# Kernel tuning notes

Measured on AMD Instinct MI355X. Metric: run time of the kernel, lower is better.

## Reference

```python
import jax, jax.numpy as jnp
import numpy as np

N = 262144
LOC_ENC_LEN = 60
NUM_WEIGHTS = 8
INDIM = 32
OUTDIM = 32
HIDDEN = 32
NEG_SLOPE = 0.01  # nn.LeakyReLU default


def _linear_init(key, fan_in, fan_out):
    # torch nn.Linear default: U(-1/sqrt(fan_in), 1/sqrt(fan_in))
    kw, kb = jax.random.split(key)
    bound = 1.0 / np.sqrt(fan_in)
    w = jax.random.uniform(kw, (fan_in, fan_out), jnp.float32, -bound, bound)
    b = jax.random.uniform(kb, (fan_out,), jnp.float32, -bound, bound)
    return w, b


def setup_inputs() -> dict:
    key = jax.random.key(0)
    ks = jax.random.split(key, 10)
    rel_loc_feat = jax.random.normal(ks[0], (N, LOC_ENC_LEN), jnp.float32)
    feat = jax.random.normal(ks[1], (N, INDIM), jnp.float32)
    dims = [LOC_ENC_LEN, HIDDEN, HIDDEN, HIDDEN, HIDDEN, HIDDEN, NUM_WEIGHTS]
    params = {}
    for i in range(6):
        w, b = _linear_init(ks[2 + i], dims[i], dims[i + 1])
        params[f'sn_w{i}'] = w
        params[f'sn_b{i}'] = b
    # weights_bank: kaiming_normal on [num_weights, indim*outdim] -> std = sqrt(2/fan_in), fan_in = indim*outdim
    std = np.sqrt(2.0 / (INDIM * OUTDIM))
    params['bank'] = jax.random.normal(ks[9], (NUM_WEIGHTS, INDIM * OUTDIM), jnp.float32) * std
    return {'rel_loc_feat': rel_loc_feat, 'feat': feat, **params}


def _score_net(x, ws, bs):
    # 5 Linear+LeakyReLU blocks, then final Linear (no activation)
    for i in range(5):
        x = x @ ws[i] + bs[i]
        x = jnp.where(x >= 0, x, NEG_SLOPE * x)
    return x @ ws[5] + bs[5]


def reference(rel_loc_feat, feat,
              sn_w0, sn_b0, sn_w1, sn_b1, sn_w2, sn_b2,
              sn_w3, sn_b3, sn_w4, sn_b4, sn_w5, sn_b5, bank):
    ws = [sn_w0, sn_w1, sn_w2, sn_w3, sn_w4, sn_w5]
    bs = [sn_b0, sn_b1, sn_b2, sn_b3, sn_b4, sn_b5]
    logits = _score_net(rel_loc_feat, ws, bs)          # [N, num_weights]
    coeff = jax.nn.softmax(logits, axis=-1)            # [N, num_weights]
    # per-point weight matrix: [N, indim*outdim] -> [N, indim, outdim]
    weights = (coeff @ bank).reshape(coeff.shape[0], INDIM, OUTDIM)
    # per-point matmul: feat[:, None] @ weights -> squeeze
    out = jnp.einsum('ni,nio->no', feat, weights)      # [N, outdim]
    return out
```

## Files before the change

### kernel.cpp

```cpp
#include <hip/hip_runtime.h>
#include <stdint.h>


typedef __attribute__((ext_vector_type(8))) __bf16 bf16x8;
typedef __attribute__((ext_vector_type(4))) float f32x4;

union FragU { uint32_t u[4]; bf16x8 v; uint4 q; };

__device__ __forceinline__ unsigned short f2bf(float f) {
    union { float f; uint32_t i; } v; v.f = f;
    return (unsigned short)((v.i + 0x7FFFu + ((v.i >> 16) & 1u)) >> 16);
}
__device__ __forceinline__ float bf2f(uint32_t u16) {
    union { uint32_t i; float f; } v; v.i = u16 << 16; return v.f;
}
__device__ __forceinline__ uint32_t pk2(float x, float y) {
    return (uint32_t)f2bf(x) | ((uint32_t)f2bf(y) << 16);
}
__device__ __forceinline__ int permK(int k) {
    return 4 * (k >> 3) + (k & 3) + 16 * ((k >> 2) & 1);
}
__device__ __forceinline__ f32x4 MF(bf16x8 a, bf16x8 b, f32x4 c) {
    return __builtin_amdgcn_mfma_f32_16x16x32_bf16(a, b, c, 0, 0, 0);
}


struct WPf { const float* p[13]; };

__global__ void pc_prep(WPf wp, uint32_t* __restrict__ ws) {
    int idx = blockIdx.x * blockDim.x + threadIdx.x;
    if (idx >= 10240) return;
    if (idx < 7424) {
        int layer, t, chunk = 0, lane, d; const float* w; bool perm;
        int r = idx;
        if (r < 1024) { chunk = r >> 9; r &= 511; t = r >> 8; r &= 255; lane = r >> 2; d = r & 3;
                        layer = 0; w = wp.p[0]; perm = false; }
        else if (r < 3072) { r -= 1024; layer = 1 + (r >> 9); r &= 511; t = r >> 8; r &= 255;
                             lane = r >> 2; d = r & 3; w = wp.p[2 * layer]; perm = true; }
        else if (r < 3328) { r -= 3072; layer = 5; t = 0; lane = r >> 2; d = r & 3;
                             w = wp.p[10]; perm = true; }
        else { r -= 3328; int bk = r >> 9; r &= 511; t = r >> 8; r &= 255; lane = r >> 2; d = r & 3;
               layer = -1; w = wp.p[12] + bk * 1024; perm = false; }
        int gq = lane >> 4, m = t * 16 + (lane & 15);
        uint32_t o = 0;
        #pragma unroll
        for (int e = 0; e < 2; ++e) {
            int kf = 8 * gq + 2 * d + e;
            float v = 0.f;
            if (layer == -1) {
                v = w[kf * 32 + m];
            } else {
                int ks = perm ? permK(kf) : (chunk * 32 + kf);
                if (layer == 0)      { if (ks < 60) v = w[ks * 32 + m]; }
                else if (layer == 5) { if (m < 8)   v = w[ks * 8 + m]; }
                else                 v = w[ks * 32 + m];
            }
            o |= ((uint32_t)f2bf(v)) << (16 * e);
        }
        ws[idx] = o;
    } else if (idx < 9984) {
        int r = idx - 7424; int L = r >> 9; r &= 511; int t = r >> 8; r &= 255;
        int lane = r >> 2, rr = r & 3;
        ((float*)ws)[idx] = wp.p[2 * L + 1][t * 16 + 4 * (lane >> 4) + rr];
    } else {
        int r = idx - 9984; int lane = r >> 2, rr = r & 3;
        int m = 4 * (lane >> 4) + rr;
        ((float*)ws)[idx] = (m < 8) ? wp.p[11][m] : 0.f;
    }
}

#define IT 8

__global__ __launch_bounds__(256, 2) void pc_main(
    const float* __restrict__ rel, const float* __restrict__ feat,
    const uint32_t* __restrict__ wsu, float* __restrict__ out)
{
    const int lane = threadIdx.x & 63;
    const int wv = threadIdx.x >> 6;
    const int g = lane >> 4;
    const int n16 = lane & 15;

    bf16x8 A0[2][2], A14[4][2], A5, AB[8][2];
    f32x4 Bi[5][2], Bi5;
    {
        #pragma unroll
        for (int c = 0; c < 2; ++c)
            #pragma unroll
            for (int t = 0; t < 2; ++t) {
                FragU f; f.q = ((const uint4*)(wsu + (c * 2 + t) * 256))[lane];
                A0[c][t] = f.v;
            }
        #pragma unroll
        for (int L = 0; L < 4; ++L)
            #pragma unroll
            for (int t = 0; t < 2; ++t) {
                FragU f; f.q = ((const uint4*)(wsu + 1024 + L * 512 + t * 256))[lane];
                A14[L][t] = f.v;
            }
        { FragU f; f.q = ((const uint4*)(wsu + 3072))[lane]; A5 = f.v; }
        #pragma unroll
        for (int k = 0; k < 8; ++k)
            #pragma unroll
            for (int t = 0; t < 2; ++t) {
                FragU f; f.q = ((const uint4*)(wsu + 3328 + (k * 2 + t) * 256))[lane];
                AB[k][t] = f.v;
            }
        const float* bw = (const float*)wsu;
        #pragma unroll
        for (int L = 0; L < 5; ++L)
            #pragma unroll
            for (int t = 0; t < 2; ++t) {
                float4 b = ((const float4*)(bw + 7424 + L * 512 + t * 256))[lane];
                Bi[L][t][0] = b.x; Bi[L][t][1] = b.y; Bi[L][t][2] = b.z; Bi[L][t][3] = b.w;
            }
        float4 b = ((const float4*)(bw + 9984))[lane];
        Bi5[0] = b.x; Bi5[1] = b.y; Bi5[2] = b.z; Bi5[3] = b.w;
    }

    const size_t pt0 = (size_t)(blockIdx.x * 4 + wv) * (16 * IT);

    for (int it = 0; it < IT; ++it) {
        const size_t n = pt0 + (size_t)it * 16 + n16;

        const float* rrow = rel + n * 60;
        float4 ra = *(const float4*)(rrow + 8 * g);
        float4 rb = *(const float4*)(rrow + 8 * g + 4);
        float4 rc = *(const float4*)(rrow + 32 + 8 * g);
        float4 rd = make_float4(0.f, 0.f, 0.f, 0.f);
        if (g < 3) rd = *(const float4*)(rrow + 36 + 8 * g);
        FragU b0, b1;
        b0.u[0] = pk2(ra.x, ra.y); b0.u[1] = pk2(ra.z, ra.w);
        b0.u[2] = pk2(rb.x, rb.y); b0.u[3] = pk2(rb.z, rb.w);
        b1.u[0] = pk2(rc.x, rc.y); b1.u[1] = pk2(rc.z, rc.w);
        b1.u[2] = pk2(rd.x, rd.y); b1.u[3] = pk2(rd.z, rd.w);

        f32x4 t0 = Bi[0][0], t1 = Bi[0][1];
        t0 = MF(A0[0][0], b0.v, t0); t1 = MF(A0[0][1], b0.v, t1);
        t0 = MF(A0[1][0], b1.v, t0); t1 = MF(A0[1][1], b1.v, t1);

        #pragma unroll
        for (int L = 0; L < 5; ++L) {
            FragU bx;
            #pragma unroll
            for (int r = 0; r < 4; ++r) {
                t0[r] = fmaxf(t0[r], 0.f) + 0.01f * fminf(t0[r], 0.f);
                t1[r] = fmaxf(t1[r], 0.f) + 0.01f * fminf(t1[r], 0.f);
            }
            bx.u[0] = pk2(t0[0], t0[1]); bx.u[1] = pk2(t0[2], t0[3]);
            bx.u[2] = pk2(t1[0], t1[1]); bx.u[3] = pk2(t1[2], t1[3]);
            if (L < 4) {
                f32x4 n0 = Bi[L + 1][0], n1 = Bi[L + 1][1];
                n0 = MF(A14[L][0], bx.v, n0);
                n1 = MF(A14[L][1], bx.v, n1);
                t0 = n0; t1 = n1;
            } else {
                t0 = MF(A5, bx.v, Bi5);
            }
        }

        float m4 = fmaxf(fmaxf(t0[0], t0[1]), fmaxf(t0[2], t0[3]));
        float m8 = fmaxf(m4, __shfl_xor(m4, 16, 64));
        float e0 = __expf(t0[0] - m8), e1 = __expf(t0[1] - m8);
        float e2 = __expf(t0[2] - m8), e3 = __expf(t0[3] - m8);
        float s4 = e0 + e1 + e2 + e3;
        float s8 = s4 + __shfl_xor(s4, 16, 64);
        float inv = 1.0f / s8;
        uint32_t pc01 = pk2(e0 * inv, e1 * inv);
        uint32_t pc23 = pk2(e2 * inv, e3 * inv);
        uint32_t q01 = (uint32_t)__builtin_amdgcn_ds_bpermute(n16 * 4, (int)pc01);
        uint32_t q23 = (uint32_t)__builtin_amdgcn_ds_bpermute(n16 * 4, (int)pc23);
        uint32_t q45 = (uint32_t)__builtin_amdgcn_ds_bpermute((n16 + 16) * 4, (int)pc01);
        uint32_t q67 = (uint32_t)__builtin_amdgcn_ds_bpermute((n16 + 16) * 4, (int)pc23);
        float cw[8] = { bf2f(q01 & 0xffff), bf2f(q01 >> 16),
                        bf2f(q23 & 0xffff), bf2f(q23 >> 16),
                        bf2f(q45 & 0xffff), bf2f(q45 >> 16),
                        bf2f(q67 & 0xffff), bf2f(q67 >> 16) };

        const float* frow = feat + n * 32 + 8 * g;
        float4 fa = *(const float4*)frow;
        float4 fb = *(const float4*)(frow + 4);
        FragU bf_;
        bf_.u[0] = pk2(fa.x, fa.y); bf_.u[1] = pk2(fa.z, fa.w);
        bf_.u[2] = pk2(fb.x, fb.y); bf_.u[3] = pk2(fb.z, fb.w);

        f32x4 o0 = {0.f, 0.f, 0.f, 0.f}, o1 = {0.f, 0.f, 0.f, 0.f};
        #pragma unroll
        for (int k = 0; k < 8; ++k) {
            f32x4 z = {0.f, 0.f, 0.f, 0.f};
            f32x4 u0 = MF(AB[k][0], bf_.v, z);
            f32x4 u1 = MF(AB[k][1], bf_.v, z);
            #pragma unroll
            for (int r = 0; r < 4; ++r) { o0[r] += cw[k] * u0[r]; o1[r] += cw[k] * u1[r]; }
        }

        float* orow = out + n * 32;
        *(float4*)(orow + 4 * g)      = make_float4(o0[0], o0[1], o0[2], o0[3]);
        *(float4*)(orow + 16 + 4 * g) = make_float4(o1[0], o1[1], o1[2], o1[3]);
    }
}

extern "C" void kernel_launch(void* const* d_in, const int* in_sizes, int n_in,
                              void* d_out, int out_size, void* d_ws, size_t ws_size,
                              hipStream_t stream)
{
    const float* rel = (const float*)d_in[0];
    const float* feat = (const float*)d_in[1];
    WPf wp;
    for (int i = 0; i < 13; ++i) wp.p[i] = (const float*)d_in[2 + i];
    uint32_t* ws = (uint32_t*)d_ws;
    float* out = (float*)d_out;

    const int npts = in_sizes[0] / 60;
    const int nwaves = npts / (16 * IT);
    const int nblocks = nwaves / 4;

    hipLaunchKernelGGL(pc_prep, dim3(40), dim3(256), 0, stream, wp, ws);
    hipLaunchKernelGGL(pc_main, dim3(nblocks), dim3(256), 0, stream, rel, feat, ws, out);
}
```

Measured before the change: 163.2 us.

## Stage weight fragments in LDS and process two 16-point tiles per iteration

```diff
diff --git a/kernel.cpp b/kernel.cpp
--- a/kernel.cpp
+++ b/kernel.cpp
@@ -69,134 +69,168 @@
     }
 }
 
-#define IT 8
+#define IT 4
 
 __global__ __launch_bounds__(256, 2) void pc_main(
     const float* __restrict__ rel, const float* __restrict__ feat,
     const uint32_t* __restrict__ wsu, float* __restrict__ out)
 {
+    __shared__ __align__(16) uint32_t W[10240];
+    {
+        uint4* s4 = (uint4*)W;
+        const uint4* g4 = (const uint4*)wsu;
+        #pragma unroll
+        for (int i = 0; i < 10; ++i) s4[threadIdx.x + 256 * i] = g4[threadIdx.x + 256 * i];
+    }
+    __syncthreads();
+
     const int lane = threadIdx.x & 63;
     const int wv = threadIdx.x >> 6;
     const int g = lane >> 4;
     const int n16 = lane & 15;
 
-    bf16x8 A0[2][2], A14[4][2], A5, AB[8][2];
     f32x4 Bi[5][2], Bi5;
+    #pragma unroll
+    for (int L = 0; L < 5; ++L)
+        #pragma unroll
+        for (int t = 0; t < 2; ++t) {
+            float4 b = ((const float4*)(W + 7424 + L * 512 + t * 256))[lane];
+            Bi[L][t][0] = b.x; Bi[L][t][1] = b.y; Bi[L][t][2] = b.z; Bi[L][t][3] = b.w;
+        }
     {
-        #pragma unroll
-        for (int c = 0; c < 2; ++c)
-            #pragma unroll
-            for (int t = 0; t < 2; ++t) {
-                FragU f; f.q = ((const uint4*)(wsu + (c * 2 + t) * 256))[lane];
-                A0[c][t] = f.v;
-            }
-        #pragma unroll
-        for (int L = 0; L < 4; ++L)
-            #pragma unroll
-            for (int t = 0; t < 2; ++t) {
-                FragU f; f.q = ((const uint4*)(wsu + 1024 + L * 512 + t * 256))[lane];
-                A14[L][t] = f.v;
-            }
-        { FragU f; f.q = ((const uint4*)(wsu + 3072))[lane]; A5 = f.v; }
-        #pragma unroll
-        for (int k = 0; k < 8; ++k)
-            #pragma unroll
-            for (int t = 0; t < 2; ++t) {
-                FragU f; f.q = ((const uint4*)(wsu + 3328 + (k * 2 + t) * 256))[lane];
-                AB[k][t] = f.v;
-            }
-        const float* bw = (const float*)wsu;
-        #pragma unroll
-        for (int L = 0; L < 5; ++L)
-            #pragma unroll
-            for (int t = 0; t < 2; ++t) {
-                float4 b = ((const float4*)(bw + 7424 + L * 512 + t * 256))[lane];
-                Bi[L][t][0] = b.x; Bi[L][t][1] = b.y; Bi[L][t][2] = b.z; Bi[L][t][3] = b.w;
-            }
-        float4 b = ((const float4*)(bw + 9984))[lane];
+        float4 b = ((const float4*)(W + 9984))[lane];
         Bi5[0] = b.x; Bi5[1] = b.y; Bi5[2] = b.z; Bi5[3] = b.w;
     }
 
-    const size_t pt0 = (size_t)(blockIdx.x * 4 + wv) * (16 * IT);
+    const size_t pt0 = (size_t)(blockIdx.x * 4 + wv) * (32 * IT);
+
+    #define LDF(off) ({ FragU _f; _f.q = ((const uint4*)(W + (off)))[lane]; _f.v; })
 
     for (int it = 0; it < IT; ++it) {
-        const size_t n = pt0 + (size_t)it * 16 + n16;
-
-        const float* rrow = rel + n * 60;
-        float4 ra = *(const float4*)(rrow + 8 * g);
-        float4 rb = *(const float4*)(rrow + 8 * g + 4);
-        float4 rc = *(const float4*)(rrow + 32 + 8 * g);
-        float4 rd = make_float4(0.f, 0.f, 0.f, 0.f);
-        if (g < 3) rd = *(const float4*)(rrow + 36 + 8 * g);
-        FragU b0, b1;
-        b0.u[0] = pk2(ra.x, ra.y); b0.u[1] = pk2(ra.z, ra.w);
-        b0.u[2] = pk2(rb.x, rb.y); b0.u[3] = pk2(rb.z, rb.w);
-        b1.u[0] = pk2(rc.x, rc.y); b1.u[1] = pk2(rc.z, rc.w);
-        b1.u[2] = pk2(rd.x, rd.y); b1.u[3] = pk2(rd.z, rd.w);
-
-        f32x4 t0 = Bi[0][0], t1 = Bi[0][1];
-        t0 = MF(A0[0][0], b0.v, t0); t1 = MF(A0[0][1], b0.v, t1);
-        t0 = MF(A0[1][0], b1.v, t0); t1 = MF(A0[1][1], b1.v, t1);
-
-        #pragma unroll
-        for (int L = 0; L < 5; ++L) {
-            FragU bx;
-            #pragma unroll
-            for (int r = 0; r < 4; ++r) {
-                t0[r] = fmaxf(t0[r], 0.f) + 0.01f * fminf(t0[r], 0.f);
-                t1[r] = fmaxf(t1[r], 0.f) + 0.01f * fminf(t1[r], 0.f);
-            }
-            bx.u[0] = pk2(t0[0], t0[1]); bx.u[1] = pk2(t0[2], t0[3]);
-            bx.u[2] = pk2(t1[0], t1[1]); bx.u[3] = pk2(t1[2], t1[3]);
-            if (L < 4) {
-                f32x4 n0 = Bi[L + 1][0], n1 = Bi[L + 1][1];
-                n0 = MF(A14[L][0], bx.v, n0);
-                n1 = MF(A14[L][1], bx.v, n1);
-                t0 = n0; t1 = n1;
-            } else {
-                t0 = MF(A5, bx.v, Bi5);
-            }
-        }
-
-        float m4 = fmaxf(fmaxf(t0[0], t0[1]), fmaxf(t0[2], t0[3]));
-        float m8 = fmaxf(m4, __shfl_xor(m4, 16, 64));
-        float e0 = __expf(t0[0] - m8), e1 = __expf(t0[1] - m8);
-        float e2 = __expf(t0[2] - m8), e3 = __expf(t0[3] - m8);
-        float s4 = e0 + e1 + e2 + e3;
-        float s8 = s4 + __shfl_xor(s4, 16, 64);
-        float inv = 1.0f / s8;
-        uint32_t pc01 = pk2(e0 * inv, e1 * inv);
-        uint32_t pc23 = pk2(e2 * inv, e3 * inv);
-        uint32_t q01 = (uint32_t)__builtin_amdgcn_ds_bpermute(n16 * 4, (int)pc01);
-        uint32_t q23 = (uint32_t)__builtin_amdgcn_ds_bpermute(n16 * 4, (int)pc23);
-        uint32_t q45 = (uint32_t)__builtin_amdgcn_ds_bpermute((n16 + 16) * 4, (int)pc01);
-        uint32_t q67 = (uint32_t)__builtin_amdgcn_ds_bpermute((n16 + 16) * 4, (int)pc23);
-        float cw[8] = { bf2f(q01 & 0xffff), bf2f(q01 >> 16),
-                        bf2f(q23 & 0xffff), bf2f(q23 >> 16),
-                        bf2f(q45 & 0xffff), bf2f(q45 >> 16),
-                        bf2f(q67 & 0xffff), bf2f(q67 >> 16) };
-
-        const float* frow = feat + n * 32 + 8 * g;
-        float4 fa = *(const float4*)frow;
-        float4 fb = *(const float4*)(frow + 4);
-        FragU bf_;
-        bf_.u[0] = pk2(fa.x, fa.y); bf_.u[1] = pk2(fa.z, fa.w);
-        bf_.u[2] = pk2(fb.x, fb.y); bf_.u[3] = pk2(fb.z, fb.w);
-
-        f32x4 o0 = {0.f, 0.f, 0.f, 0.f}, o1 = {0.f, 0.f, 0.f, 0.f};
+        const size_t nA = pt0 + (size_t)it * 32 + n16;
+
+        FragU c0[2], c1[2];
+        #pragma unroll
+        for (int q = 0; q < 2; ++q) {
+            const float* rrow = rel + (nA + 16 * q) * 60;
+            float4 ra = *(const float4*)(rrow + 8 * g);
+            float4 rb = *(const float4*)(rrow + 8 * g + 4);
+            float4 rc = *(const float4*)(rrow + 32 + 8 * g);
+            float4 rd = make_float4(0.f, 0.f, 0.f, 0.f);
+            if (g < 3) rd = *(const float4*)(rrow + 36 + 8 * g);
+            c0[q].u[0] = pk2(ra.x, ra.y); c0[q].u[1] = pk2(ra.z, ra.w);
+            c0[q].u[2] = pk2(rb.x, rb.y); c0[q].u[3] = pk2(rb.z, rb.w);
+            c1[q].u[0] = pk2(rc.x, rc.y); c1[q].u[1] = pk2(rc.z, rc.w);
+            c1[q].u[2] = pk2(rd.x, rd.y); c1[q].u[3] = pk2(rd.z, rd.w);
+        }
+
+        f32x4 t0[2], t1[2];
+        #pragma unroll
+        for (int q = 0; q < 2; ++q) { t0[q] = Bi[0][0]; t1[q] = Bi[0][1]; }
+        {
+            bf16x8 w00 = LDF(0), w01 = LDF(256), w10 = LDF(512), w11 = LDF(768);
+            #pragma unroll
+            for (int q = 0; q < 2; ++q) {
+                t0[q] = MF(w00, c0[q].v, t0[q]); t1[q] = MF(w01, c0[q].v, t1[q]);
+                t0[q] = MF(w10, c1[q].v, t0[q]); t1[q] = MF(w11, c1[q].v, t1[q]);
+            }
+        }
+
+        #pragma unroll
+        for (int L = 0; L < 4; ++L) {
+            bf16x8 wa = LDF(1024 + L * 512), wb = LDF(1024 + L * 512 + 256);
+            #pragma unroll
+            for (int q = 0; q < 2; ++q) {
+                FragU bx;
+                #pragma unroll
+                for (int r = 0; r < 4; ++r) {
+                    t0[q][r] = fmaxf(t0[q][r], 0.01f * t0[q][r]);
+                    t1[q][r] = fmaxf(t1[q][r], 0.01f * t1[q][r]);
+                }
+                bx.u[0] = pk2(t0[q][0], t0[q][1]); bx.u[1] = pk2(t0[q][2], t0[q][3]);
+                bx.u[2] = pk2(t1[q][0], t1[q][1]); bx.u[3] = pk2(t1[q][2], t1[q][3]);
+                t0[q] = MF(wa, bx.v, Bi[L + 1][0]);
+                t1[q] = MF(wb, bx.v, Bi[L + 1][1]);
+            }
+        }
+
+        {
+            bf16x8 w5 = LDF(3072);
+            #pragma unroll
+            for (int q = 0; q < 2; ++q) {
+                FragU bx;
+                #pragma unroll
+                for (int r = 0; r < 4; ++r) {
+                    t0[q][r] = fmaxf(t0[q][r], 0.01f * t0[q][r]);
+                    t1[q][r] = fmaxf(t1[q][r], 0.01f * t1[q][r]);
+                }
+                bx.u[0] = pk2(t0[q][0], t0[q][1]); bx.u[1] = pk2(t0[q][2], t0[q][3]);
+                bx.u[2] = pk2(t1[q][0], t1[q][1]); bx.u[3] = pk2(t1[q][2], t1[q][3]);
+                t0[q] = MF(w5, bx.v, Bi5);
+            }
+        }
+
+        float cw[2][8];
+        #pragma unroll
+        for (int q = 0; q < 2; ++q) {
+            float m4 = fmaxf(fmaxf(t0[q][0], t0[q][1]), fmaxf(t0[q][2], t0[q][3]));
+            float m8 = fmaxf(m4, __shfl_xor(m4, 16, 64));
+            float e0 = __expf(t0[q][0] - m8), e1 = __expf(t0[q][1] - m8);
+            float e2 = __expf(t0[q][2] - m8), e3 = __expf(t0[q][3] - m8);
+            float s4 = e0 + e1 + e2 + e3;
+            float s8 = s4 + __shfl_xor(s4, 16, 64);
+            float inv = 1.0f / s8;
+            uint32_t p01 = pk2(e0 * inv, e1 * inv);
+            uint32_t p23 = pk2(e2 * inv, e3 * inv);
+            uint32_t q01 = (uint32_t)__builtin_amdgcn_ds_bpermute(n16 * 4, (int)p01);
+            uint32_t q23 = (uint32_t)__builtin_amdgcn_ds_bpermute(n16 * 4, (int)p23);
+            uint32_t q45 = (uint32_t)__builtin_amdgcn_ds_bpermute((n16 + 16) * 4, (int)p01);
+            uint32_t q67 = (uint32_t)__builtin_amdgcn_ds_bpermute((n16 + 16) * 4, (int)p23);
+            cw[q][0] = bf2f(q01 & 0xffff); cw[q][1] = bf2f(q01 >> 16);
+            cw[q][2] = bf2f(q23 & 0xffff); cw[q][3] = bf2f(q23 >> 16);
+            cw[q][4] = bf2f(q45 & 0xffff); cw[q][5] = bf2f(q45 >> 16);
+            cw[q][6] = bf2f(q67 & 0xffff); cw[q][7] = bf2f(q67 >> 16);
+        }
+
+        FragU bf_[2];
+        #pragma unroll
+        for (int q = 0; q < 2; ++q) {
+            const float* frow = feat + (nA + 16 * q) * 32 + 8 * g;
+            float4 fa = *(const float4*)frow;
+            float4 fb = *(const float4*)(frow + 4);
+            bf_[q].u[0] = pk2(fa.x, fa.y); bf_[q].u[1] = pk2(fa.z, fa.w);
+            bf_[q].u[2] = pk2(fb.x, fb.y); bf_[q].u[3] = pk2(fb.z, fb.w);
+        }
+        f32x4 o0[2], o1[2];
+        #pragma unroll
+        for (int q = 0; q < 2; ++q) {
+            o0[q] = (f32x4){0.f, 0.f, 0.f, 0.f};
+            o1[q] = (f32x4){0.f, 0.f, 0.f, 0.f};
+        }
         #pragma unroll
         for (int k = 0; k < 8; ++k) {
-            f32x4 z = {0.f, 0.f, 0.f, 0.f};
-            f32x4 u0 = MF(AB[k][0], bf_.v, z);
-            f32x4 u1 = MF(AB[k][1], bf_.v, z);
-            #pragma unroll
-            for (int r = 0; r < 4; ++r) { o0[r] += cw[k] * u0[r]; o1[r] += cw[k] * u1[r]; }
-        }
-
-        float* orow = out + n * 32;
-        *(float4*)(orow + 4 * g)      = make_float4(o0[0], o0[1], o0[2], o0[3]);
-        *(float4*)(orow + 16 + 4 * g) = make_float4(o1[0], o1[1], o1[2], o1[3]);
-    }
+            bf16x8 wk0 = LDF(3328 + k * 512), wk1 = LDF(3328 + k * 512 + 256);
+            #pragma unroll
+            for (int q = 0; q < 2; ++q) {
+                f32x4 z = {0.f, 0.f, 0.f, 0.f};
+                f32x4 u0 = MF(wk0, bf_[q].v, z);
+                f32x4 u1 = MF(wk1, bf_[q].v, z);
+                #pragma unroll
+                for (int r = 0; r < 4; ++r) {
+                    o0[q][r] += cw[q][k] * u0[r];
+                    o1[q][r] += cw[q][k] * u1[r];
+                }
+            }
+        }
+
+        #pragma unroll
+        for (int q = 0; q < 2; ++q) {
+            float* orow = out + (nA + 16 * q) * 32;
+            *(float4*)(orow + 4 * g)      = make_float4(o0[q][0], o0[q][1], o0[q][2], o0[q][3]);
+            *(float4*)(orow + 16 + 4 * g) = make_float4(o1[q][0], o1[q][1], o1[q][2], o1[q][3]);
+        }
+    }
+    #undef LDF
 }
 
 extern "C" void kernel_launch(void* const* d_in, const int* in_sizes, int n_in,
@@ -211,8 +245,7 @@
     float* out = (float*)d_out;
 
     const int npts = in_sizes[0] / 60;
-    const int nwaves = npts / (16 * IT);
-    const int nblocks = nwaves / 4;
+    const int nblocks = npts / (32 * IT * 4);
 
     hipLaunchKernelGGL(pc_prep, dim3(40), dim3(256), 0, stream, wp, ws);
     hipLaunchKernelGGL(pc_main, dim3(nblocks), dim3(256), 0, stream, rel, feat, ws, out);
```

Measured after the change: 160.2 us. No clear change (-1.9%).

## Stage MFMA weight fragments in LDS to cut registers and raise occupancy

Applied to the files above, without the earlier changes.

```diff
diff --git a/kernel.cpp b/kernel.cpp
--- a/kernel.cpp
+++ b/kernel.cpp
@@ -69,56 +69,44 @@
     }
 }
 
-#define IT 8
-
-__global__ __launch_bounds__(256, 2) void pc_main(
+#define IT 2
+
+__global__ __launch_bounds__(256, 4) void pc_main(
     const float* __restrict__ rel, const float* __restrict__ feat,
     const uint32_t* __restrict__ wsu, float* __restrict__ out)
 {
+    __shared__ __align__(16) uint32_t W[7424];
+    {
+        uint4* s4 = (uint4*)W;
+        const uint4* g4 = (const uint4*)wsu;
+        for (int i = threadIdx.x; i < 1856; i += 256) s4[i] = g4[i];
+    }
+    __syncthreads();
+
     const int lane = threadIdx.x & 63;
     const int wv = threadIdx.x >> 6;
     const int g = lane >> 4;
     const int n16 = lane & 15;
 
-    bf16x8 A0[2][2], A14[4][2], A5, AB[8][2];
+    const float* bw = (const float*)wsu;
     f32x4 Bi[5][2], Bi5;
+    #pragma unroll
+    for (int L = 0; L < 5; ++L)
+        #pragma unroll
+        for (int t = 0; t < 2; ++t) {
+            float4 b = ((const float4*)(bw + 7424 + L * 512 + t * 256))[lane];
+            Bi[L][t][0] = b.x; Bi[L][t][1] = b.y; Bi[L][t][2] = b.z; Bi[L][t][3] = b.w;
+        }
     {
-        #pragma unroll
-        for (int c = 0; c < 2; ++c)
-            #pragma unroll
-            for (int t = 0; t < 2; ++t) {
-                FragU f; f.q = ((const uint4*)(wsu + (c * 2 + t) * 256))[lane];
-                A0[c][t] = f.v;
-            }
-        #pragma unroll
-        for (int L = 0; L < 4; ++L)
-            #pragma unroll
-            for (int t = 0; t < 2; ++t) {
-                FragU f; f.q = ((const uint4*)(wsu + 1024 + L * 512 + t * 256))[lane];
-                A14[L][t] = f.v;
-            }
-        { FragU f; f.q = ((const uint4*)(wsu + 3072))[lane]; A5 = f.v; }
-        #pragma unroll
-        for (int k = 0; k < 8; ++k)
-            #pragma unroll
-            for (int t = 0; t < 2; ++t) {
-                FragU f; f.q = ((const uint4*)(wsu + 3328 + (k * 2 + t) * 256))[lane];
-                AB[k][t] = f.v;
-            }
-        const float* bw = (const float*)wsu;
-        #pragma unroll
-        for (int L = 0; L < 5; ++L)
-            #pragma unroll
-            for (int t = 0; t < 2; ++t) {
-                float4 b = ((const float4*)(bw + 7424 + L * 512 + t * 256))[lane];
-                Bi[L][t][0] = b.x; Bi[L][t][1] = b.y; Bi[L][t][2] = b.z; Bi[L][t][3] = b.w;
-            }
         float4 b = ((const float4*)(bw + 9984))[lane];
         Bi5[0] = b.x; Bi5[1] = b.y; Bi5[2] = b.z; Bi5[3] = b.w;
     }
 
     const size_t pt0 = (size_t)(blockIdx.x * 4 + wv) * (16 * IT);
 
+    #define LDF(off) ({ FragU _f; _f.q = ((const uint4*)(W + (off)))[lane]; _f.v; })
+
+    #pragma unroll
     for (int it = 0; it < IT; ++it) {
         const size_t n = pt0 + (size_t)it * 16 + n16;
 
@@ -128,6 +116,10 @@
         float4 rc = *(const float4*)(rrow + 32 + 8 * g);
         float4 rd = make_float4(0.f, 0.f, 0.f, 0.f);
         if (g < 3) rd = *(const float4*)(rrow + 36 + 8 * g);
+        const float* frow = feat + n * 32 + 8 * g;
+        float4 fa = *(const float4*)frow;
+        float4 fb = *(const float4*)(frow + 4);
+
         FragU b0, b1;
         b0.u[0] = pk2(ra.x, ra.y); b0.u[1] = pk2(ra.z, ra.w);
         b0.u[2] = pk2(rb.x, rb.y); b0.u[3] = pk2(rb.z, rb.w);
@@ -135,27 +127,33 @@
         b1.u[2] = pk2(rd.x, rd.y); b1.u[3] = pk2(rd.z, rd.w);
 
         f32x4 t0 = Bi[0][0], t1 = Bi[0][1];
-        t0 = MF(A0[0][0], b0.v, t0); t1 = MF(A0[0][1], b0.v, t1);
-        t0 = MF(A0[1][0], b1.v, t0); t1 = MF(A0[1][1], b1.v, t1);
-
-        #pragma unroll
-        for (int L = 0; L < 5; ++L) {
+        t0 = MF(LDF(0),   b0.v, t0); t1 = MF(LDF(256), b0.v, t1);
+        t0 = MF(LDF(512), b1.v, t0); t1 = MF(LDF(768), b1.v, t1);
+
+        #pragma unroll
+        for (int L = 0; L < 4; ++L) {
             FragU bx;
             #pragma unroll
             for (int r = 0; r < 4; ++r) {
-                t0[r] = fmaxf(t0[r], 0.f) + 0.01f * fminf(t0[r], 0.f);
-                t1[r] = fmaxf(t1[r], 0.f) + 0.01f * fminf(t1[r], 0.f);
+                t0[r] = fmaxf(t0[r], 0.01f * t0[r]);
+                t1[r] = fmaxf(t1[r], 0.01f * t1[r]);
             }
             bx.u[0] = pk2(t0[0], t0[1]); bx.u[1] = pk2(t0[2], t0[3]);
             bx.u[2] = pk2(t1[0], t1[1]); bx.u[3] = pk2(t1[2], t1[3]);
-            if (L < 4) {
-                f32x4 n0 = Bi[L + 1][0], n1 = Bi[L + 1][1];
-                n0 = MF(A14[L][0], bx.v, n0);
-                n1 = MF(A14[L][1], bx.v, n1);
-                t0 = n0; t1 = n1;
-            } else {
-                t0 = MF(A5, bx.v, Bi5);
-            }
+            t0 = MF(LDF(1024 + L * 512),       bx.v, Bi[L + 1][0]);
+            t1 = MF(LDF(1024 + L * 512 + 256), bx.v, Bi[L + 1][1]);
+        }
+
+        {
+            FragU bx;
+            #pragma unroll
+            for (int r = 0; r < 4; ++r) {
+                t0[r] = fmaxf(t0[r], 0.01f * t0[r]);
+                t1[r] = fmaxf(t1[r], 0.01f * t1[r]);
+            }
+            bx.u[0] = pk2(t0[0], t0[1]); bx.u[1] = pk2(t0[2], t0[3]);
+            bx.u[2] = pk2(t1[0], t1[1]); bx.u[3] = pk2(t1[2], t1[3]);
+            t0 = MF(LDF(3072), bx.v, Bi5);
         }
 
         float m4 = fmaxf(fmaxf(t0[0], t0[1]), fmaxf(t0[2], t0[3]));
@@ -165,20 +163,17 @@
         float s4 = e0 + e1 + e2 + e3;
         float s8 = s4 + __shfl_xor(s4, 16, 64);
         float inv = 1.0f / s8;
-        uint32_t pc01 = pk2(e0 * inv, e1 * inv);
-        uint32_t pc23 = pk2(e2 * inv, e3 * inv);
-        uint32_t q01 = (uint32_t)__builtin_amdgcn_ds_bpermute(n16 * 4, (int)pc01);
-        uint32_t q23 = (uint32_t)__builtin_amdgcn_ds_bpermute(n16 * 4, (int)pc23);
-        uint32_t q45 = (uint32_t)__builtin_amdgcn_ds_bpermute((n16 + 16) * 4, (int)pc01);
-        uint32_t q67 = (uint32_t)__builtin_amdgcn_ds_bpermute((n16 + 16) * 4, (int)pc23);
+        uint32_t p01 = pk2(e0 * inv, e1 * inv);
+        uint32_t p23 = pk2(e2 * inv, e3 * inv);
+        uint32_t q01 = (uint32_t)__builtin_amdgcn_ds_bpermute(n16 * 4, (int)p01);
+        uint32_t q23 = (uint32_t)__builtin_amdgcn_ds_bpermute(n16 * 4, (int)p23);
+        uint32_t q45 = (uint32_t)__builtin_amdgcn_ds_bpermute((n16 + 16) * 4, (int)p01);
+        uint32_t q67 = (uint32_t)__builtin_amdgcn_ds_bpermute((n16 + 16) * 4, (int)p23);
         float cw[8] = { bf2f(q01 & 0xffff), bf2f(q01 >> 16),
                         bf2f(q23 & 0xffff), bf2f(q23 >> 16),
                         bf2f(q45 & 0xffff), bf2f(q45 >> 16),
                         bf2f(q67 & 0xffff), bf2f(q67 >> 16) };
 
-        const float* frow = feat + n * 32 + 8 * g;
-        float4 fa = *(const float4*)frow;
-        float4 fb = *(const float4*)(frow + 4);
         FragU bf_;
         bf_.u[0] = pk2(fa.x, fa.y); bf_.u[1] = pk2(fa.z, fa.w);
         bf_.u[2] = pk2(fb.x, fb.y); bf_.u[3] = pk2(fb.z, fb.w);
@@ -187,16 +182,20 @@
         #pragma unroll
         for (int k = 0; k < 8; ++k) {
             f32x4 z = {0.f, 0.f, 0.f, 0.f};
-            f32x4 u0 = MF(AB[k][0], bf_.v, z);
-            f32x4 u1 = MF(AB[k][1], bf_.v, z);
+            f32x4 u0 = MF(LDF(3328 + k * 512),       bf_.v, z);
+            f32x4 u1 = MF(LDF(3328 + k * 512 + 256), bf_.v, z);
             #pragma unroll
-            for (int r = 0; r < 4; ++r) { o0[r] += cw[k] * u0[r]; o1[r] += cw[k] * u1[r]; }
+            for (int r = 0; r < 4; ++r) {
+                o0[r] += cw[k] * u0[r];
+                o1[r] += cw[k] * u1[r];
+            }
         }
 
         float* orow = out + n * 32;
         *(float4*)(orow + 4 * g)      = make_float4(o0[0], o0[1], o0[2], o0[3]);
         *(float4*)(orow + 16 + 4 * g) = make_float4(o1[0], o1[1], o1[2], o1[3]);
     }
+    #undef LDF
 }
 
 extern "C" void kernel_launch(void* const* d_in, const int* in_sizes, int n_in,
@@ -211,8 +210,7 @@
     float* out = (float*)d_out;
 
     const int npts = in_sizes[0] / 60;
-    const int nwaves = npts / (16 * IT);
-    const int nblocks = nwaves / 4;
+    const int nblocks = npts / (16 * IT * 4);
 
     hipLaunchKernelGGL(pc_prep, dim3(40), dim3(256), 0, stream, wp, ws);
     hipLaunchKernelGGL(pc_main, dim3(nblocks), dim3(256), 0, stream, rel, feat, ws, out);
```

Result: no change. 163.1 us (-0.1%).
